# Kernel optimization log

Measured on AMD Instinct MI355X. Metric: run time of the kernel, lower is better.

The kernel has to match this reference:

```python
import jax, jax.numpy as jnp
import numpy as np

T, B, VD, KD, HD, OD = 64, 256, 64, 64, 512, 4


def setup_inputs() -> dict:
    key = jax.random.key(0)
    ks = jax.random.split(key, 20)
    s = 0.05
    p = {}
    p["images"] = jax.random.normal(ks[0], (T, B, 3, 32, 32), jnp.float32)
    # encoder: Conv(3->32,k4,s2) ReLU Conv(32->64,k4,s2) ReLU Conv(64->64,k4,s2) Flatten Linear(256->VD)
    p["conv1_w"] = jax.random.normal(ks[1], (32, 3, 4, 4), jnp.float32) * s
    p["conv1_b"] = jnp.zeros((32,), jnp.float32)
    p["conv2_w"] = jax.random.normal(ks[2], (64, 32, 4, 4), jnp.float32) * s
    p["conv2_b"] = jnp.zeros((64,), jnp.float32)
    p["conv3_w"] = jax.random.normal(ks[3], (64, 64, 4, 4), jnp.float32) * s
    p["conv3_b"] = jnp.zeros((64,), jnp.float32)
    p["enc_w"] = jax.random.normal(ks[4], (VD, 256), jnp.float32) * s
    p["enc_b"] = jnp.zeros((VD,), jnp.float32)
    # LSTMCell(key_dim+1 -> hidden_dim), torch gate order i,f,g,o
    p["w_ih"] = jax.random.normal(ks[5], (4 * HD, KD + 1), jnp.float32) * s
    p["w_hh"] = jax.random.normal(ks[6], (4 * HD, HD), jnp.float32) * s
    p["b_ih"] = jnp.zeros((4 * HD,), jnp.float32)
    p["b_hh"] = jnp.zeros((4 * HD,), jnp.float32)
    p["out_w"] = jax.random.normal(ks[7], (OD, HD), jnp.float32) * s
    p["out_b"] = jnp.zeros((OD,), jnp.float32)
    p["gate_w"] = jax.random.normal(ks[8], (1, HD), jnp.float32) * s
    p["gate_b"] = jnp.zeros((1,), jnp.float32)
    p["key_w"] = jax.random.normal(ks[9], (KD, HD), jnp.float32) * s
    p["key_b"] = jnp.zeros((KD,), jnp.float32)
    p["conf_w"] = jax.random.normal(ks[10], (1, 1), jnp.float32)
    p["conf_b"] = jnp.zeros((1,), jnp.float32)
    return p


def reference(images, conv1_w, conv1_b, conv2_w, conv2_b, conv3_w, conv3_b,
              enc_w, enc_b, w_ih, w_hh, b_ih, b_hh, out_w, out_b,
              gate_w, gate_b, key_w, key_b, conf_w, conf_b):
    Tn, Bn = images.shape[0], images.shape[1]

    def conv(x, w, b, relu):
        y = jax.lax.conv_general_dilated(
            x, w, window_strides=(2, 2), padding='VALID',
            dimension_numbers=('NCHW', 'OIHW', 'NCHW'))
        y = y + b[None, :, None, None]
        return jax.nn.relu(y) if relu else y

    # Encode all timesteps at once (same math as per-step encoder calls).
    x = images.reshape((Tn * Bn, 3, 32, 32))
    x = conv(x, conv1_w, conv1_b, True)
    x = conv(x, conv2_w, conv2_b, True)
    x = conv(x, conv3_w, conv3_b, False)  # no ReLU after 3rd conv in Sequential
    z_all = (x.reshape((Tn * Bn, -1)) @ enc_w.T + enc_b).reshape((Tn, Bn, -1))

    def lstm(x, h, c):
        g = x @ w_ih.T + b_ih + h @ w_hh.T + b_hh
        i, f, gg, o = jnp.split(g, 4, axis=-1)
        c2 = jax.nn.sigmoid(f) * c + jax.nn.sigmoid(i) * jnp.tanh(gg)
        return jax.nn.sigmoid(o) * jnp.tanh(c2), c2

    HDn = w_hh.shape[1]
    KDn = key_w.shape[0]
    VDn = z_all.shape[-1]
    slots = jnp.arange(Tn)

    def step(carry, xs):
        hx, cx, kx, Mk, Mv = carry
        z, t = xs
        hx, cx = lstm(kx, hx, cx)
        y = hx @ out_w.T + out_b
        g = hx @ gate_w.T + gate_b          # (b,1)
        kw = hx @ key_w.T + key_b           # (b,KD)
        # content-addressed read over the (masked) growing memory
        sim = jnp.einsum('bnd,bd->bn', Mv, z)
        mask = (slots < t)[None, :]
        wk = jax.nn.softmax(jnp.where(mask, sim, -1e30), axis=-1)
        ck = jax.nn.sigmoid(sim[..., None] * conf_w[0, 0] + conf_b[0])  # (b,n,1)
        mem = jnp.concatenate([Mk, ck], axis=-1)                         # (b,n,KD+1)
        kx_att = jax.nn.sigmoid(g) * jnp.einsum('bn,bnd->bd', wk, mem)
        kx_new = jnp.where(t == 0, jnp.zeros_like(kx_att), kx_att)      # k0 at first step
        # gated write: append kw / z at slot t
        Mk = Mk.at[:, t, :].set(kw)
        Mv = Mv.at[:, t, :].set(z)
        return (hx, cx, kx_new, Mk, Mv), y

    init = (jnp.zeros((Bn, HDn), images.dtype),
            jnp.zeros((Bn, HDn), images.dtype),
            jnp.zeros((Bn, KDn + 1), images.dtype),
            jnp.zeros((Bn, Tn, KDn), images.dtype),
            jnp.zeros((Bn, Tn, VDn), images.dtype))
    _, ys = jax.lax.scan(step, init, (z_all, slots))
    return ys  # (T, B, output_dim)
```

## Files before the change

### kernel.cpp

```cpp
#include <hip/hip_runtime.h>
#include <math.h>


__device__ __forceinline__ float sigm(float x) { return 1.0f / (1.0f + expf(-x)); }

#define PREP_N (1187840 + 2048 + 1536 + 32768 + 65536 + 16384)
__global__ __launch_bounds__(256) void prep_kernel(
    const float* __restrict__ w_ih, const float* __restrict__ w_hh,
    const float* __restrict__ b_ih, const float* __restrict__ b_hh,
    const float* __restrict__ w1, const float* __restrict__ w2,
    const float* __restrict__ w3, const float* __restrict__ ew,
    float* __restrict__ WT, float* __restrict__ bsum,
    float* __restrict__ w1T, float* __restrict__ w2T,
    float* __restrict__ w3T, float* __restrict__ ewT)
{
  int i = blockIdx.x * 256 + threadIdx.x;
  if (i < 1187840) {
    const int r = i >> 11, c = i & 2047;
    float v;
    if (r < 65)       v = w_ih[(size_t)c * 65 + r];
    else if (r < 577) v = w_hh[(size_t)c * 512 + (r - 65)];
    else              v = 0.0f;
    WT[i] = v; return;
  }
  i -= 1187840;
  if (i < 2048) { bsum[i] = b_ih[i] + b_hh[i]; return; }
  i -= 2048;
  if (i < 1536) { const int r = i >> 5, oc = i & 31; w1T[i] = w1[oc * 48 + r]; return; }
  i -= 1536;
  if (i < 32768) { const int r = i >> 6, oc = i & 63; w2T[i] = w2[oc * 512 + r]; return; }
  i -= 32768;
  if (i < 65536) { const int r = i >> 6, oc = i & 63; w3T[i] = w3[oc * 1024 + r]; return; }
  i -= 65536;
  if (i < 16384) { const int k = i >> 6, d = i & 63; ewT[i] = ew[d * 256 + k]; return; }
}

#define ENT 192
__global__ __launch_bounds__(ENT) void encoder_kernel(
    const float* __restrict__ images,
    const float* __restrict__ w1T, const float* __restrict__ b1,
    const float* __restrict__ w2T, const float* __restrict__ b2,
    const float* __restrict__ w3T, const float* __restrict__ b3,
    const float* __restrict__ ewT, const float* __restrict__ eb,
    float* __restrict__ z_all)
{
  __shared__ __align__(16) float c1[7744];
  __shared__ __align__(16) float buf[3072];
  const int bid = blockIdx.x;
  const int tid = threadIdx.x;

  {
    const float4* src = (const float4*)(images + (size_t)bid * 3072);
    float4* dst = (float4*)buf;
    for (int i = tid; i < 768; i += ENT) dst[i] = src[i];
  }
  __syncthreads();

  for (int s = tid; s < 360; s += ENT) {
    const int ocg  = s & 7;
    const int pg   = s >> 3;
    const int row  = pg / 3;
    const int colg = pg - row * 3;
    const int ox0  = colg * 5;
    float acc[4][5];
    #pragma unroll
    for (int o = 0; o < 4; ++o) {
      const float bb = b1[ocg * 4 + o];
      #pragma unroll
      for (int p = 0; p < 5; ++p) acc[o][p] = bb;
    }
    #pragma unroll
    for (int ic = 0; ic < 3; ++ic) {
      #pragma unroll
      for (int ky = 0; ky < 4; ++ky) {
        const int y = 2 * row + ky;
        const float* ib = &buf[ic * 1024 + y * 32 + 2 * ox0];
        float v[12];
        #pragma unroll
        for (int i = 0; i < 6; ++i) { float2 t2 = *(const float2*)(ib + 2 * i); v[2*i] = t2.x; v[2*i+1] = t2.y; }
        float w_[4][4];
        #pragma unroll
        for (int kx = 0; kx < 4; ++kx)
          *(float4*)&w_[kx][0] = *(const float4*)(w1T + (ic * 16 + ky * 4 + kx) * 32 + ocg * 4);
        #pragma unroll
        for (int o = 0; o < 4; ++o)
          #pragma unroll
          for (int p = 0; p < 5; ++p)
            acc[o][p] += w_[0][o] * v[2*p] + w_[1][o] * v[2*p+1] + w_[2][o] * v[2*p+2] + w_[3][o] * v[2*p+3];
      }
    }
    #pragma unroll
    for (int o = 0; o < 4; ++o)
      #pragma unroll
      for (int p = 0; p < 5; ++p)
        c1[(ocg * 4 + o) * 242 + row * 16 + ox0 + p] = fmaxf(acc[o][p], 0.0f);
  }
  __syncthreads();

  {
    const int ocg = tid & 15;
    const int pg  = tid >> 4;
    const int row = pg >> 1;
    const int ox0 = (pg & 1) * 3;
    float acc[4][3];
    #pragma unroll
    for (int o = 0; o < 4; ++o) {
      const float bb = b2[ocg * 4 + o];
      acc[o][0] = bb; acc[o][1] = bb; acc[o][2] = bb;
    }
    for (int ic = 0; ic < 32; ++ic) {
      #pragma unroll
      for (int ky = 0; ky < 4; ++ky) {
        const int y = 2 * row + ky;
        const float* ib = &c1[ic * 242 + y * 16 + 2 * ox0];
        float v[8];
        #pragma unroll
        for (int i = 0; i < 4; ++i) { float2 t2 = *(const float2*)(ib + 2 * i); v[2*i] = t2.x; v[2*i+1] = t2.y; }
        float w_[4][4];
        #pragma unroll
        for (int kx = 0; kx < 4; ++kx)
          *(float4*)&w_[kx][0] = *(const float4*)(w2T + (ic * 16 + ky * 4 + kx) * 64 + ocg * 4);
        #pragma unroll
        for (int o = 0; o < 4; ++o)
          #pragma unroll
          for (int p = 0; p < 3; ++p)
            acc[o][p] += w_[0][o] * v[2*p] + w_[1][o] * v[2*p+1] + w_[2][o] * v[2*p+2] + w_[3][o] * v[2*p+3];
      }
    }
    __syncthreads();
    #pragma unroll
    for (int o = 0; o < 4; ++o)
      #pragma unroll
      for (int p = 0; p < 3; ++p)
        buf[(ocg * 4 + o) * 38 + row * 6 + ox0 + p] = fmaxf(acc[o][p], 0.0f);
  }
  __syncthreads();

  {
    const int oc = tid & 63;
    const int kc = tid >> 6;
    const int k0 = (kc * 256) / 3, k1 = ((kc + 1) * 256) / 3;
    float acc[4] = {0.f, 0.f, 0.f, 0.f};
    for (int it = k0; it < k1; ++it) {
      const int ic = it >> 2;
      const int ky = it & 3;
      float v[2][6];
      #pragma unroll
      for (int oy = 0; oy < 2; ++oy) {
        const float* ib = &buf[ic * 38 + (2 * oy + ky) * 6];
        #pragma unroll
        for (int i = 0; i < 3; ++i) { float2 t2 = *(const float2*)(ib + 2 * i); v[oy][2*i] = t2.x; v[oy][2*i+1] = t2.y; }
      }
      float w_[4];
      #pragma unroll
      for (int kx = 0; kx < 4; ++kx) w_[kx] = w3T[(ic * 16 + ky * 4 + kx) * 64 + oc];
      #pragma unroll
      for (int p = 0; p < 4; ++p) {
        const int oy = p >> 1, ox = p & 1;
        acc[p] += w_[0] * v[oy][2*ox] + w_[1] * v[oy][2*ox+1] + w_[2] * v[oy][2*ox+2] + w_[3] * v[oy][2*ox+3];
      }
    }
    #pragma unroll
    for (int p = 0; p < 4; ++p) c1[kc * 260 + p * 64 + oc] = acc[p];
  }
  __syncthreads();

  for (int o = tid; o < 256; o += ENT) {
    const int oc = o >> 2, p = o & 3;
    c1[1024 + o] = b3[oc] + c1[p * 64 + oc] + c1[260 + p * 64 + oc] + c1[520 + p * 64 + oc];
  }
  __syncthreads();

  {
    const int d  = tid & 63;
    const int kc = tid >> 6;
    const int k0 = (kc * 256) / 3, k1 = ((kc + 1) * 256) / 3;
    float s = 0.0f;
    for (int k = k0; k < k1; ++k) s += ewT[k * 64 + d] * c1[1024 + k];
    c1[1536 + kc * 64 + d] = s;
  }
  __syncthreads();
  if (tid < 64) {
    z_all[(size_t)bid * 64 + tid] = eb[tid] + c1[1536 + tid] + c1[1600 + tid] + c1[1664 + tid];
  }
}

__global__ __launch_bounds__(256) void gram_kernel(
    const float* __restrict__ z_all, float* __restrict__ z_gram)
{
  const int b = blockIdx.x;
  const int tid = threadIdx.x;
  __shared__ float zsb[64 * 65];
  for (int i = tid; i < 4096; i += 256) {
    const int tt = i >> 6, d = i & 63;
    zsb[tt * 65 + d] = z_all[((size_t)tt * 256 + b) * 64 + d];
  }
  __syncthreads();
  const int n = tid & 63, tg = tid >> 6;
  for (int tt = tg; tt < 64; tt += 4) {
    float s = 0.0f;
    #pragma unroll
    for (int d = 0; d < 64; ++d) s += zsb[tt * 65 + d] * zsb[n * 65 + d];
    z_gram[((size_t)b * 64 + tt) * 64 + n] = s;
  }
}

__global__ __launch_bounds__(256) void gates_partial_kernel(
    const float* __restrict__ XC, const float* __restrict__ WT,
    float* __restrict__ Gp, const int kchunk, const int klog)
{
  extern __shared__ float xs[];
  const int bx  = blockIdx.x;
  const int kc  = bx & ((1 << klog) - 1);
  const int jt  = bx >> klog;
  const int tid = threadIdx.x;
  const int tj  = tid & 63, tb = tid >> 6;
  const int k0  = kc * kchunk;
  const int b0  = blockIdx.y * 16;
  const int j0  = jt * 256 + tj * 4;

  const int NS = 16 * kchunk;
  for (int i = tid; i < NS; i += 256) {
    const int b = i / kchunk, k = i - b * kchunk;
    xs[b * kchunk + k] = XC[(size_t)(b0 + b) * 580 + k0 + k];
  }
  __syncthreads();

  float acc[4][4];
  #pragma unroll
  for (int bb = 0; bb < 4; ++bb)
    #pragma unroll
    for (int jj = 0; jj < 4; ++jj) acc[bb][jj] = 0.0f;

  const float* wp = WT + (size_t)k0 * 2048 + j0;
  const float* xp = xs + tb * 4 * kchunk;
  #pragma unroll 4
  for (int k = 0; k < kchunk; ++k) {
    const float4 w = *(const float4*)(wp + (size_t)k * 2048);
    #pragma unroll
    for (int bb = 0; bb < 4; ++bb) {
      const float xv = xp[bb * kchunk + k];
      acc[bb][0] += xv * w.x; acc[bb][1] += xv * w.y;
      acc[bb][2] += xv * w.z; acc[bb][3] += xv * w.w;
    }
  }
  #pragma unroll
  for (int bb = 0; bb < 4; ++bb) {
    float4 r; r.x = acc[bb][0]; r.y = acc[bb][1]; r.z = acc[bb][2]; r.w = acc[bb][3];
    *(float4*)(Gp + ((size_t)kc * 256 + b0 + tb * 4 + bb) * 2048 + j0) = r;
  }
}

__global__ __launch_bounds__(256) void step_fused_kernel(
    const int t, const int kcn,
    const float* __restrict__ Gp, const float* __restrict__ bsum,
    float* __restrict__ C, const float* __restrict__ z_gram,
    float* __restrict__ MkT, float* __restrict__ XC, float* __restrict__ out,
    const float* __restrict__ out_w, const float* __restrict__ out_b,
    const float* __restrict__ gate_w, const float* __restrict__ gate_b,
    const float* __restrict__ key_w, const float* __restrict__ key_b,
    const float* __restrict__ conf_w, const float* __restrict__ conf_b)
{
  const int b   = blockIdx.x;
  const int tid = threadIdx.x;
  __shared__ __align__(16) float hs[512];
  __shared__ __align__(16) float wks[64];
  __shared__ __align__(16) float psum[256];
  __shared__ float sgv, kx64v;

  for (int jj = tid; jj < 512; jj += 256) {
    float gv[4];
    #pragma unroll
    for (int g = 0; g < 4; ++g) {
      float s = bsum[g * 512 + jj];
      for (int kc = 0; kc < kcn; ++kc)
        s += Gp[((size_t)kc * 256 + b) * 2048 + g * 512 + jj];
      gv[g] = s;
    }
    const size_t cidx = (size_t)b * 512 + jj;
    const float c2v = sigm(gv[1]) * C[cidx] + sigm(gv[0]) * tanhf(gv[2]);
    C[cidx] = c2v;
    const float h = sigm(gv[3]) * tanhf(c2v);
    hs[jj] = h;
    XC[(size_t)b * 580 + 65 + jj] = h;
  }
  __syncthreads();

  const int wv = tid >> 6, lane = tid & 63;
  for (int d = wv; d < 69; d += 4) {
    const float* row = (d < 64) ? (key_w + (size_t)d * 512)
                     : (d < 68) ? (out_w + (size_t)(d - 64) * 512)
                                : gate_w;
    float a = 0.0f;
    #pragma unroll
    for (int k = 0; k < 8; ++k) a += hs[lane + k * 64] * row[lane + k * 64];
    #pragma unroll
    for (int m = 32; m > 0; m >>= 1) a += __shfl_xor(a, m);
    if (lane == 0) {
      if (d < 64)      MkT[(size_t)b * 4096 + d * 64 + t] = a + key_b[d];
      else if (d < 68) out[(size_t)t * 1024 + b * 4 + (d - 64)] = a + out_b[d - 64];
      else             sgv = sigm(a + gate_b[0]);
    }
  }
  __syncthreads();

  if (t == 0) {
    if (tid < 65) XC[(size_t)b * 580 + tid] = 0.0f;
    return;
  }

  if (tid < 64) {
    const int n = tid;
    const float sim = z_gram[((size_t)b * 64 + t) * 64 + n];
    const bool valid = (n < t);
    float mx = valid ? sim : -3.0e38f;
    #pragma unroll
    for (int m = 32; m > 0; m >>= 1) mx = fmaxf(mx, __shfl_xor(mx, m));
    const float p = valid ? expf(sim - mx) : 0.0f;
    float sum = p;
    #pragma unroll
    for (int m = 32; m > 0; m >>= 1) sum += __shfl_xor(sum, m);
    const float wk = p / sum;
    wks[n] = wk;
    float kc = wk * sigm(sim * conf_w[0] + conf_b[0]);
    #pragma unroll
    for (int m = 32; m > 0; m >>= 1) kc += __shfl_xor(kc, m);
    if (n == 0) kx64v = kc;
  }
  __syncthreads();

  {
    const int d = tid >> 2, q = tid & 3;
    const float* mr = MkT + (size_t)b * 4096 + d * 64 + q * 16;
    const float* wr = wks + q * 16;
    float a = 0.0f;
    #pragma unroll
    for (int i = 0; i < 4; ++i) {
      const float4 m4 = *(const float4*)(mr + 4 * i);
      const float4 w4 = *(const float4*)(wr + 4 * i);
      a += m4.x * w4.x + m4.y * w4.y + m4.z * w4.z + m4.w * w4.w;
    }
    psum[tid] = a;
  }
  __syncthreads();
  if (tid < 64) {
    XC[(size_t)b * 580 + tid] = sgv * (psum[tid * 4] + psum[tid * 4 + 1] + psum[tid * 4 + 2] + psum[tid * 4 + 3]);
  } else if (tid == 64) {
    XC[(size_t)b * 580 + 64] = sgv * kx64v;
  }
}

extern "C" void kernel_launch(void* const* d_in, const int* in_sizes, int n_in,
                              void* d_out, int out_size, void* d_ws, size_t ws_size,
                              hipStream_t stream) {
  const float* images = (const float*)d_in[0];
  const float* w1     = (const float*)d_in[1];
  const float* b1     = (const float*)d_in[2];
  const float* w2     = (const float*)d_in[3];
  const float* b2     = (const float*)d_in[4];
  const float* w3     = (const float*)d_in[5];
  const float* b3     = (const float*)d_in[6];
  const float* ew     = (const float*)d_in[7];
  const float* eb     = (const float*)d_in[8];
  const float* w_ih   = (const float*)d_in[9];
  const float* w_hh   = (const float*)d_in[10];
  const float* b_ih   = (const float*)d_in[11];
  const float* b_hh   = (const float*)d_in[12];
  const float* out_w  = (const float*)d_in[13];
  const float* out_b  = (const float*)d_in[14];
  const float* gate_w = (const float*)d_in[15];
  const float* gate_b = (const float*)d_in[16];
  const float* key_w  = (const float*)d_in[17];
  const float* key_b  = (const float*)d_in[18];
  const float* conf_w = (const float*)d_in[19];
  const float* conf_b = (const float*)d_in[20];
  float* out = (float*)d_out;
  float* ws  = (float*)d_ws;

  float* WT     = ws;
  float* bsum   = ws + 1187840;
  float* w1T    = ws + 1189888;
  float* w2T    = ws + 1191424;
  float* w3T    = ws + 1224192;
  float* ewT    = ws + 1289728;
  float* z_all  = ws + 1306112;
  float* MkT    = ws + 2354688;
  float* C      = ws + 3403264;
  float* XC     = ws + 3534336;
  float* z_gram = ws + 3682816;
  float* Gp     = ws + 4731392;

  int kcn = 4, klog = 2, kchunk = 145;
  if (ws_size < (4731392ull + 4ull * 524288ull) * 4ull) { kcn = 2; klog = 1; kchunk = 290; }
  if (ws_size < (4731392ull + 2ull * 524288ull) * 4ull) { kcn = 1; klog = 0; kchunk = 580; }

  hipMemsetAsync(C,  0, 131072 * sizeof(float), stream);
  hipMemsetAsync(XC, 0, 148480 * sizeof(float), stream);

  prep_kernel<<<(PREP_N + 255) / 256, 256, 0, stream>>>(
      w_ih, w_hh, b_ih, b_hh, w1, w2, w3, ew, WT, bsum, w1T, w2T, w3T, ewT);

  encoder_kernel<<<16384, ENT, 0, stream>>>(images, w1T, b1, w2T, b2, w3T, b3, ewT, eb, z_all);

  gram_kernel<<<256, 256, 0, stream>>>(z_all, z_gram);

  const size_t lds_stage = (size_t)16 * kchunk * sizeof(float);
  for (int t = 0; t < 64; ++t) {
    gates_partial_kernel<<<dim3(8 * kcn, 16), 256, lds_stage, stream>>>(
        XC, WT, Gp, kchunk, klog);
    step_fused_kernel<<<256, 256, 0, stream>>>(
        t, kcn, Gp, bsum, C, z_gram, MkT, XC, out,
        out_w, out_b, gate_w, gate_b, key_w, key_b, conf_w, conf_b);
  }
}
```

Measured before the change: 4.132 ms.

## Split conv1 into channel halves to shrink LDS; retile gates GEMM with transposed x

The encoder now computes conv1 in two 16-channel halves and accumulates conv2 after each half in registers. This roughly halves the shared memory per block and should allow more resident blocks on the 16384-block launch, at the cost of an extra barrier round. The per-step gates GEMM tile changes from 16 batches x 256 columns to 32 batches x 128 columns. The staged x is stored k-major so each thread reads its four batch values with one float4 LDS load. Each weight float4 is now reused across 32 batches instead of 16, cutting global weight traffic.

```diff
diff --git a/kernel.cpp b/kernel.cpp
--- a/kernel.cpp
+++ b/kernel.cpp
@@ -36,7 +36,7 @@
 }
 
 #define ENT 192
-__global__ __launch_bounds__(ENT) void encoder_kernel(
+__global__ __launch_bounds__(ENT) void enc_fused_kernel(
     const float* __restrict__ images,
     const float* __restrict__ w1T, const float* __restrict__ b1,
     const float* __restrict__ w2T, const float* __restrict__ b2,
@@ -44,96 +44,98 @@
     const float* __restrict__ ewT, const float* __restrict__ eb,
     float* __restrict__ z_all)
 {
-  __shared__ __align__(16) float c1[7744];
-  __shared__ __align__(16) float buf[3072];
+  __shared__ __align__(16) float bufA[3072];
+  __shared__ __align__(16) float bufB[3872];
   const int bid = blockIdx.x;
   const int tid = threadIdx.x;
 
   {
     const float4* src = (const float4*)(images + (size_t)bid * 3072);
-    float4* dst = (float4*)buf;
+    float4* dst = (float4*)bufA;
     for (int i = tid; i < 768; i += ENT) dst[i] = src[i];
   }
   __syncthreads();
 
-  for (int s = tid; s < 360; s += ENT) {
-    const int ocg  = s & 7;
-    const int pg   = s >> 3;
-    const int row  = pg / 3;
-    const int colg = pg - row * 3;
-    const int ox0  = colg * 5;
-    float acc[4][5];
-    #pragma unroll
-    for (int o = 0; o < 4; ++o) {
-      const float bb = b1[ocg * 4 + o];
-      #pragma unroll
-      for (int p = 0; p < 5; ++p) acc[o][p] = bb;
-    }
-    #pragma unroll
-    for (int ic = 0; ic < 3; ++ic) {
+  const int ocg2 = tid & 15;
+  const int pg2  = tid >> 4;
+  const int row2 = pg2 >> 1;
+  const int ox02 = (pg2 & 1) * 3;
+  float acc2[4][3];
+  #pragma unroll
+  for (int o = 0; o < 4; ++o) {
+    const float bb = b2[ocg2 * 4 + o];
+    acc2[o][0] = bb; acc2[o][1] = bb; acc2[o][2] = bb;
+  }
+
+  for (int half = 0; half < 2; ++half) {
+    for (int s = tid; s < 180; s += ENT) {
+      const int ocg  = s & 3;
+      const int pg   = s >> 2;
+      const int row  = pg / 3;
+      const int colg = pg - row * 3;
+      const int ox0  = colg * 5;
+      float acc[4][5];
+      #pragma unroll
+      for (int o = 0; o < 4; ++o) {
+        const float bb = b1[half * 16 + ocg * 4 + o];
+        #pragma unroll
+        for (int p = 0; p < 5; ++p) acc[o][p] = bb;
+      }
+      #pragma unroll
+      for (int ic = 0; ic < 3; ++ic) {
+        #pragma unroll
+        for (int ky = 0; ky < 4; ++ky) {
+          const int y = 2 * row + ky;
+          const float* ib = &bufA[ic * 1024 + y * 32 + 2 * ox0];
+          float v[12];
+          #pragma unroll
+          for (int i = 0; i < 6; ++i) { float2 t2 = *(const float2*)(ib + 2 * i); v[2*i] = t2.x; v[2*i+1] = t2.y; }
+          float w_[4][4];
+          #pragma unroll
+          for (int kx = 0; kx < 4; ++kx)
+            *(float4*)&w_[kx][0] = *(const float4*)(w1T + (ic * 16 + ky * 4 + kx) * 32 + half * 16 + ocg * 4);
+          #pragma unroll
+          for (int o = 0; o < 4; ++o)
+            #pragma unroll
+            for (int p = 0; p < 5; ++p)
+              acc[o][p] += w_[0][o] * v[2*p] + w_[1][o] * v[2*p+1] + w_[2][o] * v[2*p+2] + w_[3][o] * v[2*p+3];
+        }
+      }
+      #pragma unroll
+      for (int o = 0; o < 4; ++o)
+        #pragma unroll
+        for (int p = 0; p < 5; ++p)
+          bufB[(ocg * 4 + o) * 242 + row * 16 + ox0 + p] = fmaxf(acc[o][p], 0.0f);
+    }
+    __syncthreads();
+
+    for (int icl = 0; icl < 16; ++icl) {
       #pragma unroll
       for (int ky = 0; ky < 4; ++ky) {
-        const int y = 2 * row + ky;
-        const float* ib = &buf[ic * 1024 + y * 32 + 2 * ox0];
-        float v[12];
-        #pragma unroll
-        for (int i = 0; i < 6; ++i) { float2 t2 = *(const float2*)(ib + 2 * i); v[2*i] = t2.x; v[2*i+1] = t2.y; }
-        float w_[4][4];
-        #pragma unroll
-        for (int kx = 0; kx < 4; ++kx)
-          *(float4*)&w_[kx][0] = *(const float4*)(w1T + (ic * 16 + ky * 4 + kx) * 32 + ocg * 4);
-        #pragma unroll
-        for (int o = 0; o < 4; ++o)
-          #pragma unroll
-          for (int p = 0; p < 5; ++p)
-            acc[o][p] += w_[0][o] * v[2*p] + w_[1][o] * v[2*p+1] + w_[2][o] * v[2*p+2] + w_[3][o] * v[2*p+3];
-      }
-    }
-    #pragma unroll
-    for (int o = 0; o < 4; ++o)
-      #pragma unroll
-      for (int p = 0; p < 5; ++p)
-        c1[(ocg * 4 + o) * 242 + row * 16 + ox0 + p] = fmaxf(acc[o][p], 0.0f);
-  }
-  __syncthreads();
-
-  {
-    const int ocg = tid & 15;
-    const int pg  = tid >> 4;
-    const int row = pg >> 1;
-    const int ox0 = (pg & 1) * 3;
-    float acc[4][3];
-    #pragma unroll
-    for (int o = 0; o < 4; ++o) {
-      const float bb = b2[ocg * 4 + o];
-      acc[o][0] = bb; acc[o][1] = bb; acc[o][2] = bb;
-    }
-    for (int ic = 0; ic < 32; ++ic) {
-      #pragma unroll
-      for (int ky = 0; ky < 4; ++ky) {
-        const int y = 2 * row + ky;
-        const float* ib = &c1[ic * 242 + y * 16 + 2 * ox0];
+        const int y = 2 * row2 + ky;
+        const float* ib = &bufB[icl * 242 + y * 16 + 2 * ox02];
         float v[8];
         #pragma unroll
         for (int i = 0; i < 4; ++i) { float2 t2 = *(const float2*)(ib + 2 * i); v[2*i] = t2.x; v[2*i+1] = t2.y; }
         float w_[4][4];
         #pragma unroll
         for (int kx = 0; kx < 4; ++kx)
-          *(float4*)&w_[kx][0] = *(const float4*)(w2T + (ic * 16 + ky * 4 + kx) * 64 + ocg * 4);
+          *(float4*)&w_[kx][0] = *(const float4*)(w2T + ((half * 16 + icl) * 16 + ky * 4 + kx) * 64 + ocg2 * 4);
         #pragma unroll
         for (int o = 0; o < 4; ++o)
           #pragma unroll
           for (int p = 0; p < 3; ++p)
-            acc[o][p] += w_[0][o] * v[2*p] + w_[1][o] * v[2*p+1] + w_[2][o] * v[2*p+2] + w_[3][o] * v[2*p+3];
+            acc2[o][p] += w_[0][o] * v[2*p] + w_[1][o] * v[2*p+1] + w_[2][o] * v[2*p+2] + w_[3][o] * v[2*p+3];
       }
     }
     __syncthreads();
-    #pragma unroll
-    for (int o = 0; o < 4; ++o)
-      #pragma unroll
-      for (int p = 0; p < 3; ++p)
-        buf[(ocg * 4 + o) * 38 + row * 6 + ox0 + p] = fmaxf(acc[o][p], 0.0f);
-  }
+  }
+
+  #pragma unroll
+  for (int o = 0; o < 4; ++o)
+    #pragma unroll
+    for (int p = 0; p < 3; ++p)
+      bufA[(ocg2 * 4 + o) * 37 + row2 * 6 + ox02 + p] = fmaxf(acc2[o][p], 0.0f);
   __syncthreads();
 
   {
@@ -147,7 +149,7 @@
       float v[2][6];
       #pragma unroll
       for (int oy = 0; oy < 2; ++oy) {
-        const float* ib = &buf[ic * 38 + (2 * oy + ky) * 6];
+        const float* ib = &bufA[ic * 37 + (2 * oy + ky) * 6];
         #pragma unroll
         for (int i = 0; i < 3; ++i) { float2 t2 = *(const float2*)(ib + 2 * i); v[oy][2*i] = t2.x; v[oy][2*i+1] = t2.y; }
       }
@@ -161,13 +163,13 @@
       }
     }
     #pragma unroll
-    for (int p = 0; p < 4; ++p) c1[kc * 260 + p * 64 + oc] = acc[p];
+    for (int p = 0; p < 4; ++p) bufB[kc * 260 + p * 64 + oc] = acc[p];
   }
   __syncthreads();
 
   for (int o = tid; o < 256; o += ENT) {
     const int oc = o >> 2, p = o & 3;
-    c1[1024 + o] = b3[oc] + c1[p * 64 + oc] + c1[260 + p * 64 + oc] + c1[520 + p * 64 + oc];
+    bufB[1024 + o] = b3[oc] + bufB[p * 64 + oc] + bufB[260 + p * 64 + oc] + bufB[520 + p * 64 + oc];
   }
   __syncthreads();
 
@@ -176,12 +178,12 @@
     const int kc = tid >> 6;
     const int k0 = (kc * 256) / 3, k1 = ((kc + 1) * 256) / 3;
     float s = 0.0f;
-    for (int k = k0; k < k1; ++k) s += ewT[k * 64 + d] * c1[1024 + k];
-    c1[1536 + kc * 64 + d] = s;
+    for (int k = k0; k < k1; ++k) s += ewT[k * 64 + d] * bufB[1024 + k];
+    bufB[1536 + kc * 64 + d] = s;
   }
   __syncthreads();
   if (tid < 64) {
-    z_all[(size_t)bid * 64 + tid] = eb[tid] + c1[1536 + tid] + c1[1600 + tid] + c1[1664 + tid];
+    z_all[(size_t)bid * 64 + tid] = eb[tid] + bufB[1536 + tid] + bufB[1600 + tid] + bufB[1664 + tid];
   }
 }
 
@@ -214,34 +216,33 @@
   const int kc  = bx & ((1 << klog) - 1);
   const int jt  = bx >> klog;
   const int tid = threadIdx.x;
-  const int tj  = tid & 63, tb = tid >> 6;
+  const int tj  = tid & 31, tb = tid >> 5;
   const int k0  = kc * kchunk;
-  const int b0  = blockIdx.y * 16;
-  const int j0  = jt * 256 + tj * 4;
-
-  const int NS = 16 * kchunk;
+  const int b0  = blockIdx.y * 32;
+  const int j0  = jt * 128 + tj * 4;
+
+  const int NS = 32 * kchunk;
   for (int i = tid; i < NS; i += 256) {
-    const int b = i / kchunk, k = i - b * kchunk;
-    xs[b * kchunk + k] = XC[(size_t)(b0 + b) * 580 + k0 + k];
+    const int k = i >> 5, b = i & 31;
+    xs[k * 32 + b] = XC[(size_t)(b0 + b) * 580 + k0 + k];
   }
   __syncthreads();
 
   float acc[4][4];
   #pragma unroll
-  for (int bb = 0; bb < 4; ++bb)
-    #pragma unroll
-    for (int jj = 0; jj < 4; ++jj) acc[bb][jj] = 0.0f;
+  for (int bb = 0; bb < 4; ++bb) { acc[bb][0]=0.f; acc[bb][1]=0.f; acc[bb][2]=0.f; acc[bb][3]=0.f; }
 
   const float* wp = WT + (size_t)k0 * 2048 + j0;
-  const float* xp = xs + tb * 4 * kchunk;
+  const float* xp = xs + tb * 4;
   #pragma unroll 4
   for (int k = 0; k < kchunk; ++k) {
     const float4 w = *(const float4*)(wp + (size_t)k * 2048);
+    const float4 x = *(const float4*)(xp + k * 32);
+    const float xv[4] = {x.x, x.y, x.z, x.w};
     #pragma unroll
     for (int bb = 0; bb < 4; ++bb) {
-      const float xv = xp[bb * kchunk + k];
-      acc[bb][0] += xv * w.x; acc[bb][1] += xv * w.y;
-      acc[bb][2] += xv * w.z; acc[bb][3] += xv * w.w;
+      acc[bb][0] += xv[bb] * w.x; acc[bb][1] += xv[bb] * w.y;
+      acc[bb][2] += xv[bb] * w.z; acc[bb][3] += xv[bb] * w.w;
     }
   }
   #pragma unroll
@@ -322,10 +323,10 @@
     for (int m = 32; m > 0; m >>= 1) sum += __shfl_xor(sum, m);
     const float wk = p / sum;
     wks[n] = wk;
-    float kc = wk * sigm(sim * conf_w[0] + conf_b[0]);
-    #pragma unroll
-    for (int m = 32; m > 0; m >>= 1) kc += __shfl_xor(kc, m);
-    if (n == 0) kx64v = kc;
+    float kcv = wk * sigm(sim * conf_w[0] + conf_b[0]);
+    #pragma unroll
+    for (int m = 32; m > 0; m >>= 1) kcv += __shfl_xor(kcv, m);
+    if (n == 0) kx64v = kcv;
   }
   __syncthreads();
 
@@ -400,13 +401,14 @@
   prep_kernel<<<(PREP_N + 255) / 256, 256, 0, stream>>>(
       w_ih, w_hh, b_ih, b_hh, w1, w2, w3, ew, WT, bsum, w1T, w2T, w3T, ewT);
 
-  encoder_kernel<<<16384, ENT, 0, stream>>>(images, w1T, b1, w2T, b2, w3T, b3, ewT, eb, z_all);
+  enc_fused_kernel<<<16384, ENT, 0, stream>>>(
+      images, w1T, b1, w2T, b2, w3T, b3, ewT, eb, z_all);
 
   gram_kernel<<<256, 256, 0, stream>>>(z_all, z_gram);
 
-  const size_t lds_stage = (size_t)16 * kchunk * sizeof(float);
+  const size_t lds_stage = (size_t)32 * kchunk * sizeof(float);
   for (int t = 0; t < 64; ++t) {
-    gates_partial_kernel<<<dim3(8 * kcn, 16), 256, lds_stage, stream>>>(
+    gates_partial_kernel<<<dim3(16 * kcn, 8), 256, lds_stage, stream>>>(
         XC, WT, Gp, kchunk, klog);
     step_fused_kernel<<<256, 256, 0, stream>>>(
         t, kcn, Gp, bsum, C, z_gram, MkT, XC, out,
```

Result: slower. 4.496 ms (+8.8%).
